# Optimization experiments

Hardware: AMD Instinct MI355X
Metric: run time of the kernel (lower is better)

The kernel has to match this reference:

```python
import jax, jax.numpy as jnp
import numpy as np

EPS = 1e-5

def group_norm(x, num_groups, eps=EPS):
    # x: [B, C, H, W]; no affine (matches F.group_norm with weight=None)
    B, C, H, W = x.shape
    xg = x.reshape(B, num_groups, (C // num_groups) * H * W)
    mean = jnp.mean(xg, axis=-1, keepdims=True)
    var = jnp.var(xg, axis=-1, keepdims=True)
    xg = (xg - mean) * jax.lax.rsqrt(var + eps)
    return xg.reshape(B, C, H, W)

def setup_inputs() -> dict:
    key = jax.random.key(0)
    ks = jax.random.split(key, 5)
    B, C, H, W = 32, 256, 32, 32
    # kaiming-uniform-ish scale for linear weights
    bound = 1.0 / np.sqrt(C)
    x = jax.random.normal(ks[0], (B, C, H, W), dtype=jnp.float32)
    WQ = jax.random.uniform(ks[1], (C, C), jnp.float32, -bound, bound)
    WK = jax.random.uniform(ks[2], (C, C), jnp.float32, -bound, bound)
    WV = jax.random.uniform(ks[3], (C, C), jnp.float32, -bound, bound)
    Wo = jax.random.uniform(ks[4], (C, C), jnp.float32, -bound, bound)
    z = jnp.zeros((C,), jnp.float32)
    return {"x": x, "WQ": WQ, "bQ": z, "WK": WK, "bK": z,
            "WV": WV, "bV": z, "Wo": Wo, "bo": z}

def reference(x, WQ, bQ, WK, bK, WV, bV, Wo, bo):
    B, C, H, W = x.shape
    G = min(32, C)
    h = group_norm(x, G)                      # [B,C,H,W]
    h = h.reshape(B, C, H * W).transpose(0, 2, 1)  # [B, S, C], S = H*W
    q = h @ WQ + bQ
    k = h @ WK + bK
    v = h @ WV + bV
    scale = C ** (-0.5)
    attn = jnp.einsum('bsc,btc->bst', q, k) * scale   # [B,S,S]
    attn = jax.nn.softmax(attn, axis=-1)
    o = jnp.einsum('bst,btc->bsc', attn, v)           # [B,S,C]
    o = o @ Wo + bo                                   # output Nin while in [B,S,C]
    o = o.transpose(0, 2, 1).reshape(B, C, H, W)
    return x + o
```

## Files before the change

kernel.cpp:

```cpp
#include <hip/hip_runtime.h>
#include <stdint.h>

#define BB  32
#define CC  256
#define SS  1024
#define GG  32
#define GCH 8
#define EPS 1e-5f

typedef __attribute__((ext_vector_type(8))) short short8;
typedef __attribute__((ext_vector_type(4))) float f32x4;
typedef __attribute__((ext_vector_type(16))) float f32x16;
typedef unsigned short ushort;

__device__ __forceinline__ float bf2f(ushort u){
  union { unsigned int i; float f; } v; v.i = ((unsigned int)u) << 16; return v.f;
}
__device__ __forceinline__ ushort f2bf(float f){
  union { float f; unsigned int i; } v; v.f = f;
  unsigned int r = v.i + 0x7FFFu + ((v.i >> 16) & 1u);
  return (ushort)(r >> 16);
}
__device__ __forceinline__ unsigned int cvt_pk_bf16(float lo, float hi){
  unsigned int r;
  asm("v_cvt_pk_bf16_f32 %0, %1, %2" : "=v"(r) : "v"(lo), "v"(hi));
  return r;
}

typedef __attribute__((address_space(3))) unsigned int lds_uint;
typedef const __attribute__((address_space(1))) unsigned int glob_uint;
__device__ __forceinline__ void ld_lds16(const void* g, void* l){
  __builtin_amdgcn_global_load_lds((glob_uint*)g, (lds_uint*)l, 16, 0, 0);
}

__global__ __launch_bounds__(256) void sniff_k(const unsigned int* __restrict__ xw,
                                               int* __restrict__ flag)
{
  const int tid = threadIdx.x;
  unsigned int w = xw[tid];
  ushort lo = (ushort)(w & 0xFFFFu);
  int e = (lo >> 7) & 0xFF;
  int ok = (lo == 0 || (e >= 100 && e <= 130)) ? 1 : 0;
  __shared__ int cnt;
  if (tid == 0) cnt = 0;
  __syncthreads();
  atomicAdd(&cnt, ok);
  __syncthreads();
  if (tid == 0) *flag = (cnt > 192) ? 1 : 0;
}

__global__ __launch_bounds__(256) void convert_pre(
    const void* w0, const void* w1, const void* w2, const void* w3,
    const void* b0, const void* b1, const void* b2, const void* b3,
    ushort* __restrict__ WT, float* __restrict__ biasF,
    const int* __restrict__ flag)
{
  const int f = *flag;
  const int z = blockIdx.z;
  const float scl = (z == 0) ? 0.0901684400557f : 1.0f;
  const void* wsel = z==0?w0:z==1?w1:z==2?w2:w3;
  ushort* dst = WT + (long long)z * 65536;
  __shared__ ushort t[64][65];
  const int tid = threadIdx.x;
  const int tx = tid & 63, ty = tid >> 6;
  const int r0 = blockIdx.x * 64, c0 = blockIdx.y * 64;
  for (int j = 0; j < 64; j += 4){
    const int idx = (r0+ty+j)*256 + c0+tx;
    float v = f ? bf2f(((const ushort*)wsel)[idx]) : ((const float*)wsel)[idx];
    t[ty+j][tx] = f2bf(v * scl);
  }
  __syncthreads();
  for (int j = 0; j < 64; j += 4) dst[(c0+ty+j)*256 + r0+tx] = t[tx][ty+j];
  if (blockIdx.x == 0 && blockIdx.y == 0){
    const void* bsel = z==0?b0:z==1?b1:z==2?b2:b3;
    float bv = f ? bf2f(((const ushort*)bsel)[tid]) : ((const float*)bsel)[tid];
    biasF[z*256 + tid] = bv * scl;
  }
}

__global__ __launch_bounds__(256) void gn_stats(const void* __restrict__ x,
                                                float* __restrict__ stats,
                                                const int* __restrict__ flag)
{
  const int f = *flag;
  const int g = blockIdx.x, b = blockIdx.y;
  const int tid = threadIdx.x;
  const long long base = ((long long)b * CC + g * GCH) * SS;
  float sum = 0.f, ss = 0.f;
  if (f){
    const ushort* xg = (const ushort*)x + base;
    #pragma unroll
    for (int j = 0; j < 4; j++){
      uint4 u = *(const uint4*)(xg + (j*256 + tid)*8);
      const ushort* e = (const ushort*)&u;
      #pragma unroll
      for (int i = 0; i < 8; i++){ float v = bf2f(e[i]); sum += v; ss += v*v; }
    }
  } else {
    const float* xg = (const float*)x + base;
    #pragma unroll
    for (int j = 0; j < 8; j++){
      float4 v4 = *(const float4*)(xg + (j*256 + tid)*4);
      sum += v4.x+v4.y+v4.z+v4.w;
      ss  += v4.x*v4.x+v4.y*v4.y+v4.z*v4.z+v4.w*v4.w;
    }
  }
  __shared__ float red[8];
  const int lane = tid & 63, w = tid >> 6;
  #pragma unroll
  for (int o = 32; o > 0; o >>= 1){
    sum += __shfl_down(sum, o);
    ss  += __shfl_down(ss, o);
  }
  if (lane == 0){ red[w] = sum; red[4+w] = ss; }
  __syncthreads();
  if (tid == 0){
    float s1 = red[0]+red[1]+red[2]+red[3];
    float s2 = red[4]+red[5]+red[6]+red[7];
    float mean = s1 / (float)(GCH*SS);
    float var  = s2 / (float)(GCH*SS) - mean*mean;
    const int idx = b*GG + g;
    stats[idx*2]   = mean;
    stats[idx*2+1] = rsqrtf(var + EPS);
  }
}

__global__ __launch_bounds__(256) void gn_norm(const void* __restrict__ x,
                                               ushort* __restrict__ h,
                                               const float* __restrict__ stats,
                                               const int* __restrict__ flag)
{
  const int f = *flag;
  const int c0 = blockIdx.x * 64, s0 = blockIdx.y * 64, b = blockIdx.z;
  const int tid = threadIdx.x;
  __shared__ ushort T[64][72];
  const int row = tid >> 2;
  const int qr  = tid & 3;
  const int g = (c0 + row) >> 3;
  const float mean = stats[(b*GG + g)*2];
  const float rstd = stats[(b*GG + g)*2 + 1];
  const long long xrow = ((long long)b * CC + c0 + row) * SS + s0;
  if (f){
    const ushort* xr = (const ushort*)x + xrow;
    #pragma unroll
    for (int j = 0; j < 2; j++){
      const int col = qr*16 + j*8;
      uint4 u = *(const uint4*)(xr + col);
      const ushort* e = (const ushort*)&u;
      #pragma unroll
      for (int i = 0; i < 8; i++) T[row][col+i] = f2bf((bf2f(e[i]) - mean) * rstd);
    }
  } else {
    const float* xr = (const float*)x + xrow;
    #pragma unroll
    for (int j = 0; j < 4; j++){
      const int col = qr*16 + j*4;
      float4 v4 = *(const float4*)(xr + col);
      T[row][col+0] = f2bf((v4.x - mean) * rstd);
      T[row][col+1] = f2bf((v4.y - mean) * rstd);
      T[row][col+2] = f2bf((v4.z - mean) * rstd);
      T[row][col+3] = f2bf((v4.w - mean) * rstd);
    }
  }
  __syncthreads();
  #pragma unroll
  for (int pass = 0; pass < 2; pass++){
    const int sr = pass*32 + (tid >> 3);
    const int cl = (tid & 7) * 8;
    ushort tmp[8];
    #pragma unroll
    for (int e = 0; e < 8; e++) tmp[e] = T[cl+e][sr];
    *(uint4*)(&h[((long long)b * SS + s0 + sr) * CC + c0 + cl]) = *(const uint4*)tmp;
  }
}

template<int MODE>
__global__ __launch_bounds__(256) void gemm128(
    const ushort* __restrict__ A,
    const ushort* __restrict__ BT,
    ushort* __restrict__ Cmat,
    int lda, int ldb, int ldc, int K,
    long long sA, long long sB, long long sC,
    const float* __restrict__ biasF,
    const void* __restrict__ xres,
    void* __restrict__ outp,
    ushort* __restrict__ vTp,
    long long xoff,
    const int* __restrict__ flag)
{
  extern __shared__ __attribute__((aligned(16))) ushort smem[];
  ushort* As = smem;
  ushort* Bs = smem + 8192;
  const int tid  = threadIdx.x;
  const int lane = tid & 63;
  const int w    = tid >> 6;
  const int wr   = w >> 1, wc = w & 1;
  const int bz   = blockIdx.z;
  const int m0 = blockIdx.x * 128;
  const int n0 = blockIdx.y * 128;

  const int rr = lane & 15;
  const int hi = lane >> 4;
  const int crow = lane >> 3;
  const int pslot = lane & 7;

  f32x4 acc[4][4] = {};

  const ushort* Ab = A + (long long)bz * sA;
  const ushort* Bb = BT + (long long)bz * sB;

  for (int k0 = 0; k0 < K; k0 += 64){
    #pragma unroll
    for (int j = 0; j < 4; j++){
      const int ck = w*4 + j;
      const int r  = ck*8 + crow;
      const int s  = pslot ^ (r & 7);
      ld_lds16(Ab + (long long)(m0 + r) * lda + k0 + s*8, &As[ck * 512]);
    }
    #pragma unroll
    for (int j = 0; j < 4; j++){
      const int ck = w*4 + j;
      const int r  = ck*8 + crow;
      const int s  = pslot ^ (r & 7);
      ld_lds16(Bb + (long long)(n0 + r) * ldb + k0 + s*8, &Bs[ck * 512]);
    }
    asm volatile("s_waitcnt vmcnt(0)" ::: "memory");
    __builtin_amdgcn_sched_barrier(0);
    __syncthreads();

    #pragma unroll
    for (int kk = 0; kk < 2; kk++){
      short8 af[4], bfr[4];
      const int lbyte = kk*64 + hi*16;
      #pragma unroll
      for (int mf = 0; mf < 4; mf++){
        const int row = wr*64 + mf*16 + rr;
        af[mf] = *(const short8*)((const char*)As + row*128 + (lbyte ^ ((row & 7) << 4)));
      }
      #pragma unroll
      for (int nf = 0; nf < 4; nf++){
        const int row = wc*64 + nf*16 + rr;
        bfr[nf] = *(const short8*)((const char*)Bs + row*128 + (lbyte ^ ((row & 7) << 4)));
      }
      #pragma unroll
      for (int mf = 0; mf < 4; mf++)
        #pragma unroll
        for (int nf = 0; nf < 4; nf++)
          acc[mf][nf] = __builtin_amdgcn_mfma_f32_16x16x32_bf16(af[mf], bfr[nf], acc[mf][nf], 0, 0, 0);
    }
    __syncthreads();
  }

  const int rb = 4 * (lane >> 4);
  if (MODE == 0){
    if (bz < 2){
      ushort* Co = Cmat + (long long)bz * sC;
      #pragma unroll
      for (int mf = 0; mf < 4; mf++){
        #pragma unroll
        for (int nf = 0; nf < 4; nf++){
          const int col = n0 + wc*64 + nf*16 + rr;
          const float badd = biasF[bz*256 + col];
          #pragma unroll
          for (int r = 0; r < 4; r++){
            const int row = m0 + wr*64 + mf*16 + rb + r;
            Co[(long long)row * ldc + col] = f2bf(acc[mf][nf][r] + badd);
          }
        }
      }
    } else {
      #pragma unroll
      for (int mf = 0; mf < 4; mf++){
        #pragma unroll
        for (int nf = 0; nf < 4; nf++){
          const int col = n0 + wc*64 + nf*16 + rr;
          const float badd = biasF[512 + col];
          #pragma unroll
          for (int r = 0; r < 4; r++){
            const int row = m0 + wr*64 + mf*16 + rb + r;
            const int bL = row >> 10, s = row & 1023;
            vTp[((long long)bL * CC + col) * SS + s] = f2bf(acc[mf][nf][r] + badd);
          }
        }
      }
    }
  } else {
    const int bL = m0 >> 10;
    const int s0 = m0 & 1023;
    #pragma unroll
    for (int mf = 0; mf < 4; mf++){
      #pragma unroll
      for (int nf = 0; nf < 4; nf++){
        const int colL = wc*64 + nf*16 + rr;
        const float badd = biasF[768 + n0 + colL];
        #pragma unroll
        for (int r = 0; r < 4; r++){
          const int rowL = wr*64 + mf*16 + rb + r;
          smem[colL * 128 + rowL] = f2bf(acc[mf][nf][r] + badd);
        }
      }
    }
    __syncthreads();
    const int f = *flag;
    for (int i = tid; i < 2048; i += 256){
      const int colL = i >> 4;
      const int rowL = (i & 15) * 8;
      const long long oi = xoff + ((long long)bL * CC + n0 + colL) * SS + s0 + rowL;
      const ushort* pu = &smem[colL * 128 + rowL];
      if (f){
        const ushort* xu = (const ushort*)xres + oi;
        ushort* ou = (ushort*)outp + oi;
        ushort tmp[8];
        #pragma unroll
        for (int e = 0; e < 8; e++) tmp[e] = f2bf(bf2f(xu[e]) + bf2f(pu[e]));
        *(uint4*)ou = *(const uint4*)tmp;
      } else {
        const float* xf = (const float*)xres + oi;
        float* of = (float*)outp + oi;
        float4 a0 = *(const float4*)xf;
        float4 a1 = *(const float4*)(xf + 4);
        float4 r0, r1;
        r0.x = a0.x + bf2f(pu[0]); r0.y = a0.y + bf2f(pu[1]);
        r0.z = a0.z + bf2f(pu[2]); r0.w = a0.w + bf2f(pu[3]);
        r1.x = a1.x + bf2f(pu[4]); r1.y = a1.y + bf2f(pu[5]);
        r1.z = a1.z + bf2f(pu[6]); r1.w = a1.w + bf2f(pu[7]);
        *(float4*)of = r0;
        *(float4*)(of + 4) = r1;
      }
    }
  }
}

__global__ __launch_bounds__(512, 1) void attn_fused(
    const ushort* __restrict__ q, const ushort* __restrict__ k,
    const ushort* __restrict__ vT, ushort* __restrict__ oC)
{
  __shared__ ushort Kb[2][64 * 256];
  __shared__ ushort Vb[2][256 * 64];
  const int tid = threadIdx.x, lane = tid & 63, w = tid >> 6;
  const int l31 = lane & 31, hi2 = lane >> 5;
  const int qg = w & 3, ch = w >> 2;
  const int b = blockIdx.x, qt = blockIdx.y;

  const char* kgB = (const char*)(k + (long long)b * SS * CC);
  const char* vgB = (const char*)(vT + (long long)b * CC * SS);
  const int qrow = qt*128 + qg*32 + l31;
  const ushort* qgp = q + ((long long)b * SS + qrow) * CC + hi2*8;
  ushort* ogq = oC + ((long long)b * SS + qrow) * CC + ch*128;

  short8 qf[16];
  #pragma unroll
  for (int kk = 0; kk < 16; kk++)
    qf[kk] = *(const short8*)(qgp + kk*16);

  f32x16 Oa[4] = {};
  float mrow = -1e30f, lrow = 0.0f;

  #define STAGE(buf, t0)                                                        \
  {                                                                             \
    _Pragma("unroll")                                                           \
    for (int j = 0; j < 4; j++){                                                \
      const int ck = j*8 + w;                                                   \
      const int tr = ck*2 + (lane >> 5);                                        \
      const int xb = ((lane & 31) * 16) ^ ((tr & 31) << 4);                     \
      ld_lds16(kgB + (long long)((t0) + tr) * 512 + xb, &Kb[buf][ck * 512]);    \
    }                                                                           \
    _Pragma("unroll")                                                           \
    for (int j = 0; j < 4; j++){                                                \
      const int ck = j*8 + w;                                                   \
      const int vr = ck*2 + (lane >> 5);                                        \
      const int u  = (lane & 31) ^ ((vr & 7) << 2);                             \
      const int vc = vr*4 + (u & 3);                                            \
      const int tb = (u >> 2) * 16;                                             \
      ld_lds16(vgB + (long long)vc * 2048 + (t0)*2 + tb, &Vb[buf][ck * 512]);   \
    }                                                                           \
  }

  STAGE(0, 0);
  asm volatile("s_waitcnt vmcnt(0)" ::: "memory");
  __builtin_amdgcn_sched_barrier(0);
  __syncthreads();

  const int coff = hi2 * 16;
  const int kswz = l31 << 4;

  for (int t = 0; t < 16; t++){
    const int cur = t & 1;
    if (t < 15) STAGE(cur ^ 1, (t+1)*64);

    f32x16 Sa0 = {}, Sa1 = {};
    __builtin_amdgcn_s_setprio(1);
    #pragma unroll
    for (int kk = 0; kk < 16; kk++){
      const int off = kk*32 + coff;
      short8 ka0 = *(const short8*)((const char*)&Kb[cur][0] + l31*512 + (off ^ kswz));
      short8 ka1 = *(const short8*)((const char*)&Kb[cur][0] + (32 + l31)*512 + (off ^ kswz));
      Sa0 = __builtin_amdgcn_mfma_f32_32x32x16_bf16(ka0, qf[kk], Sa0, 0, 0, 0);
      Sa1 = __builtin_amdgcn_mfma_f32_32x32x16_bf16(ka1, qf[kk], Sa1, 0, 0, 0);
    }
    __builtin_amdgcn_s_setprio(0);

    float mx = Sa0[0];
    #pragma unroll
    for (int r = 1; r < 16; r++) mx = fmaxf(mx, Sa0[r]);
    #pragma unroll
    for (int r = 0; r < 16; r++) mx = fmaxf(mx, Sa1[r]);
    mx = fmaxf(mx, __shfl_xor(mx, 32));
    if (!__all(mx <= mrow + 8.0f)){
      const float mn = fmaxf(mrow, mx);
      const float sc = __builtin_amdgcn_exp2f(mrow - mn);
      mrow = mn;
      lrow *= sc;
      #pragma unroll
      for (int nf = 0; nf < 4; nf++)
        #pragma unroll
        for (int r = 0; r < 16; r++) Oa[nf][r] *= sc;
    }
    float rs = 0.0f;
    #pragma unroll
    for (int r = 0; r < 16; r++){
      Sa0[r] = __builtin_amdgcn_exp2f(Sa0[r] - mrow); rs += Sa0[r];
      Sa1[r] = __builtin_amdgcn_exp2f(Sa1[r] - mrow); rs += Sa1[r];
    }
    rs += __shfl_xor(rs, 32);
    lrow += rs;

    __builtin_amdgcn_s_setprio(1);
    #pragma unroll
    for (int g = 0; g < 4; g++){
      unsigned int b0, b1, b2, b3;
      if (g < 2){
        b0 = cvt_pk_bf16(Sa0[(g&1)*8+0], Sa0[(g&1)*8+1]);
        b1 = cvt_pk_bf16(Sa0[(g&1)*8+2], Sa0[(g&1)*8+3]);
        b2 = cvt_pk_bf16(Sa0[(g&1)*8+4], Sa0[(g&1)*8+5]);
        b3 = cvt_pk_bf16(Sa0[(g&1)*8+6], Sa0[(g&1)*8+7]);
      } else {
        b0 = cvt_pk_bf16(Sa1[(g&1)*8+0], Sa1[(g&1)*8+1]);
        b1 = cvt_pk_bf16(Sa1[(g&1)*8+2], Sa1[(g&1)*8+3]);
        b2 = cvt_pk_bf16(Sa1[(g&1)*8+4], Sa1[(g&1)*8+5]);
        b3 = cvt_pk_bf16(Sa1[(g&1)*8+6], Sa1[(g&1)*8+7]);
      }
      unsigned int s0 = (unsigned int)__shfl_xor((int)b0, 32);
      unsigned int s1 = (unsigned int)__shfl_xor((int)b1, 32);
      unsigned int s2 = (unsigned int)__shfl_xor((int)b2, 32);
      unsigned int s3 = (unsigned int)__shfl_xor((int)b3, 32);
      union { uint4 u; short8 s; } pw;
      pw.u.x = hi2 ? s2 : b0;
      pw.u.y = hi2 ? s3 : b1;
      pw.u.z = hi2 ? b2 : s0;
      pw.u.w = hi2 ? b3 : s1;
      const short8 pb = pw.s;
      const int G = g*2 + hi2;
      #pragma unroll
      for (int nf = 0; nf < 4; nf++){
        const int c = ch*128 + nf*32 + l31;
        const int vr = c >> 2;
        const int slot = (((G << 2) | (c & 3)) ^ ((vr & 7) << 2));
        short8 va = *(const short8*)((const char*)&Vb[cur][0] + vr*512 + slot*16);
        Oa[nf] = __builtin_amdgcn_mfma_f32_32x32x16_bf16(va, pb, Oa[nf], 0, 0, 0);
      }
    }
    __builtin_amdgcn_s_setprio(0);

    asm volatile("s_waitcnt vmcnt(0)" ::: "memory");
    __builtin_amdgcn_sched_barrier(0);
    __syncthreads();
  }
  #undef STAGE

  const float inv = 1.0f / lrow;
  #pragma unroll
  for (int nf = 0; nf < 4; nf++){
    #pragma unroll
    for (int g = 0; g < 4; g++){
      uint2 ov;
      ov.x = cvt_pk_bf16(Oa[nf][g*4+0] * inv, Oa[nf][g*4+1] * inv);
      ov.y = cvt_pk_bf16(Oa[nf][g*4+2] * inv, Oa[nf][g*4+3] * inv);
      *(uint2*)(ogq + nf*32 + g*8 + hi2*4) = ov;
    }
  }
}

extern "C" void kernel_launch(void* const* d_in, const int* in_sizes, int n_in,
                              void* d_out, int out_size, void* d_ws, size_t ws_size,
                              hipStream_t stream)
{
  (void)in_sizes; (void)n_in; (void)out_size;
  const void* x  = d_in[0];
  const void* WQ = d_in[1];
  const void* bQ = d_in[2];
  const void* WK = d_in[3];
  const void* bK = d_in[4];
  const void* WV = d_in[5];
  const void* bV = d_in[6];
  const void* Wo = d_in[7];
  const void* bo = d_in[8];

  const long long NE  = (long long)BB * SS * CC;
  const long long SC  = (long long)SS * CC;

  uint8_t* base = (uint8_t*)d_ws;
  int* flag          = (int*)base;
  float* biasF       = (float*)(base + 256);
  float* stats       = (float*)(base + 256 + 4096);
  ushort* WT         = (ushort*)(base + 256 + 4096 + 8192);
  ushort* h          = WT + 4 * 65536;

  const long long fixedB = 256 + 4096 + 8192 + 4LL*65536*2 + NE*2;
  int CB = 1;
  for (int c = 32; c >= 1; c >>= 1){
    if (fixedB + 4LL * c * SC * 2 <= (long long)ws_size){ CB = c; break; }
  }

  ushort* q  = h + NE;
  ushort* k  = q + (long long)CB * SC;
  ushort* vT = k + (long long)CB * SC;
  ushort* oC = vT + (long long)CB * SC;

  dim3 blk(256);
  const size_t shmem = 32768;

  sniff_k<<<1, blk, 0, stream>>>((const unsigned int*)x, flag);
  convert_pre<<<dim3(4, 4, 4), blk, 0, stream>>>(WQ, WK, WV, Wo, bQ, bK, bV, bo, WT, biasF, flag);
  gn_stats<<<dim3(GG, BB), blk, 0, stream>>>(x, stats, flag);
  gn_norm<<<dim3(4, 16, BB), blk, 0, stream>>>(x, h, stats, flag);

  for (int c0 = 0; c0 < BB; c0 += CB){
    const ushort* hC = h + (long long)c0 * SC;
    gemm128<0><<<dim3(CB*8, 2, 3), blk, shmem, stream>>>(
        hC, WT, q, CC, CC, CC, CC,
        0LL, 65536LL, (long long)CB * SC,
        biasF, nullptr, nullptr, vT, 0LL, flag);
    attn_fused<<<dim3(CB, 8), dim3(512), 0, stream>>>(q, k, vT, oC);
    gemm128<3><<<dim3(CB*8, 2, 1), blk, shmem, stream>>>(
        oC, WT + 3*65536, nullptr, CC, CC, SS, CC,
        0LL, 0LL, 0LL,
        biasF, x, d_out, nullptr, (long long)c0 * SC, flag);
  }
}
```

Before: 151.2 us.

## Split attention work across key halves instead of channel halves, merge via LDS

The attention kernel's two wave halves now each process half of every 64-key tile (32 keys) across all 256 output channels, instead of each computing all 64 keys' scores and splitting channels. This removes the duplicated QK^T MFMA work and the duplicated exp/max work across the two channel halves. The cost is double the O accumulator registers per wave (8 f32x16 fragments). There is also a final split-softmax merge: one half writes its partial O, max and sum to LDS, reusing the K/V buffers, and the other half combines and stores them. Higher register pressure could hurt scheduling.

```diff
diff --git a/kernel.cpp b/kernel.cpp
--- a/kernel.cpp
+++ b/kernel.cpp
@@ -337,6 +337,8 @@
 {
   __shared__ ushort Kb[2][64 * 256];
   __shared__ ushort Vb[2][256 * 64];
+  __shared__ float  Mb[8][32];
+  __shared__ float  Lb[8][32];
   const int tid = threadIdx.x, lane = tid & 63, w = tid >> 6;
   const int l31 = lane & 31, hi2 = lane >> 5;
   const int qg = w & 3, ch = w >> 2;
@@ -346,14 +348,14 @@
   const char* vgB = (const char*)(vT + (long long)b * CC * SS);
   const int qrow = qt*128 + qg*32 + l31;
   const ushort* qgp = q + ((long long)b * SS + qrow) * CC + hi2*8;
-  ushort* ogq = oC + ((long long)b * SS + qrow) * CC + ch*128;
+  ushort* ogq = oC + ((long long)b * SS + qrow) * CC;
 
   short8 qf[16];
   #pragma unroll
   for (int kk = 0; kk < 16; kk++)
     qf[kk] = *(const short8*)(qgp + kk*16);
 
-  f32x16 Oa[4] = {};
+  f32x16 Oa[8] = {};
   float mrow = -1e30f, lrow = 0.0f;
 
   #define STAGE(buf, t0)                                                        \
@@ -383,28 +385,25 @@
 
   const int coff = hi2 * 16;
   const int kswz = l31 << 4;
+  const int krow = ch*32 + l31;
 
   for (int t = 0; t < 16; t++){
     const int cur = t & 1;
     if (t < 15) STAGE(cur ^ 1, (t+1)*64);
 
-    f32x16 Sa0 = {}, Sa1 = {};
+    f32x16 Sa = {};
     __builtin_amdgcn_s_setprio(1);
     #pragma unroll
     for (int kk = 0; kk < 16; kk++){
       const int off = kk*32 + coff;
-      short8 ka0 = *(const short8*)((const char*)&Kb[cur][0] + l31*512 + (off ^ kswz));
-      short8 ka1 = *(const short8*)((const char*)&Kb[cur][0] + (32 + l31)*512 + (off ^ kswz));
-      Sa0 = __builtin_amdgcn_mfma_f32_32x32x16_bf16(ka0, qf[kk], Sa0, 0, 0, 0);
-      Sa1 = __builtin_amdgcn_mfma_f32_32x32x16_bf16(ka1, qf[kk], Sa1, 0, 0, 0);
+      short8 ka = *(const short8*)((const char*)&Kb[cur][0] + krow*512 + (off ^ kswz));
+      Sa = __builtin_amdgcn_mfma_f32_32x32x16_bf16(ka, qf[kk], Sa, 0, 0, 0);
     }
     __builtin_amdgcn_s_setprio(0);
 
-    float mx = Sa0[0];
-    #pragma unroll
-    for (int r = 1; r < 16; r++) mx = fmaxf(mx, Sa0[r]);
-    #pragma unroll
-    for (int r = 0; r < 16; r++) mx = fmaxf(mx, Sa1[r]);
+    float mx = Sa[0];
+    #pragma unroll
+    for (int r = 1; r < 16; r++) mx = fmaxf(mx, Sa[r]);
     mx = fmaxf(mx, __shfl_xor(mx, 32));
     if (!__all(mx <= mrow + 8.0f)){
       const float mn = fmaxf(mrow, mx);
@@ -412,34 +411,25 @@
       mrow = mn;
       lrow *= sc;
       #pragma unroll
-      for (int nf = 0; nf < 4; nf++)
+      for (int nf = 0; nf < 8; nf++)
         #pragma unroll
         for (int r = 0; r < 16; r++) Oa[nf][r] *= sc;
     }
     float rs = 0.0f;
     #pragma unroll
     for (int r = 0; r < 16; r++){
-      Sa0[r] = __builtin_amdgcn_exp2f(Sa0[r] - mrow); rs += Sa0[r];
-      Sa1[r] = __builtin_amdgcn_exp2f(Sa1[r] - mrow); rs += Sa1[r];
+      Sa[r] = __builtin_amdgcn_exp2f(Sa[r] - mrow); rs += Sa[r];
     }
     rs += __shfl_xor(rs, 32);
     lrow += rs;
 
     __builtin_amdgcn_s_setprio(1);
     #pragma unroll
-    for (int g = 0; g < 4; g++){
-      unsigned int b0, b1, b2, b3;
-      if (g < 2){
-        b0 = cvt_pk_bf16(Sa0[(g&1)*8+0], Sa0[(g&1)*8+1]);
-        b1 = cvt_pk_bf16(Sa0[(g&1)*8+2], Sa0[(g&1)*8+3]);
-        b2 = cvt_pk_bf16(Sa0[(g&1)*8+4], Sa0[(g&1)*8+5]);
-        b3 = cvt_pk_bf16(Sa0[(g&1)*8+6], Sa0[(g&1)*8+7]);
-      } else {
-        b0 = cvt_pk_bf16(Sa1[(g&1)*8+0], Sa1[(g&1)*8+1]);
-        b1 = cvt_pk_bf16(Sa1[(g&1)*8+2], Sa1[(g&1)*8+3]);
-        b2 = cvt_pk_bf16(Sa1[(g&1)*8+4], Sa1[(g&1)*8+5]);
-        b3 = cvt_pk_bf16(Sa1[(g&1)*8+6], Sa1[(g&1)*8+7]);
-      }
+    for (int g = 0; g < 2; g++){
+      unsigned int b0 = cvt_pk_bf16(Sa[g*8+0], Sa[g*8+1]);
+      unsigned int b1 = cvt_pk_bf16(Sa[g*8+2], Sa[g*8+3]);
+      unsigned int b2 = cvt_pk_bf16(Sa[g*8+4], Sa[g*8+5]);
+      unsigned int b3 = cvt_pk_bf16(Sa[g*8+6], Sa[g*8+7]);
       unsigned int s0 = (unsigned int)__shfl_xor((int)b0, 32);
       unsigned int s1 = (unsigned int)__shfl_xor((int)b1, 32);
       unsigned int s2 = (unsigned int)__shfl_xor((int)b2, 32);
@@ -450,10 +440,10 @@
       pw.u.z = hi2 ? b2 : s0;
       pw.u.w = hi2 ? b3 : s1;
       const short8 pb = pw.s;
-      const int G = g*2 + hi2;
-      #pragma unroll
-      for (int nf = 0; nf < 4; nf++){
-        const int c = ch*128 + nf*32 + l31;
+      const int G = ch*4 + g*2 + hi2;
+      #pragma unroll
+      for (int nf = 0; nf < 8; nf++){
+        const int c = nf*32 + l31;
         const int vr = c >> 2;
         const int slot = (((G << 2) | (c & 3)) ^ ((vr & 7) << 2));
         short8 va = *(const short8*)((const char*)&Vb[cur][0] + vr*512 + slot*16);
@@ -468,15 +458,39 @@
   }
   #undef STAGE
 
-  const float inv = 1.0f / lrow;
-  #pragma unroll
-  for (int nf = 0; nf < 4; nf++){
-    #pragma unroll
-    for (int g = 0; g < 4; g++){
-      uint2 ov;
-      ov.x = cvt_pk_bf16(Oa[nf][g*4+0] * inv, Oa[nf][g*4+1] * inv);
-      ov.y = cvt_pk_bf16(Oa[nf][g*4+2] * inv, Oa[nf][g*4+3] * inv);
-      *(uint2*)(ogq + nf*32 + g*8 + hi2*4) = ov;
+  float* Ob = (qg < 2) ? (float*)&Kb[qg][0] : (float*)&Vb[qg - 2][0];
+  if (ch == 1){
+    #pragma unroll
+    for (int nf = 0; nf < 8; nf++){
+      #pragma unroll
+      for (int r = 0; r < 16; r++){
+        const int c = nf*32 + (r & 3) + 8*(r >> 2) + 4*hi2;
+        Ob[c*32 + l31] = Oa[nf][r];
+      }
+    }
+    if (hi2 == 0){ Mb[w][l31] = mrow; Lb[w][l31] = lrow; }
+  }
+  __syncthreads();
+  if (ch == 0){
+    const float m2 = Mb[w + 4][l31], l2 = Lb[w + 4][l31];
+    const float mx = fmaxf(mrow, m2);
+    const float f1 = __builtin_amdgcn_exp2f(mrow - mx);
+    const float f2 = __builtin_amdgcn_exp2f(m2 - mx);
+    const float inv = 1.0f / (f1*lrow + f2*l2);
+    const float a1 = f1 * inv, a2 = f2 * inv;
+    #pragma unroll
+    for (int nf = 0; nf < 8; nf++){
+      #pragma unroll
+      for (int g = 0; g < 4; g++){
+        float o0 = Oa[nf][g*4+0]*a1 + Ob[(nf*32 + g*8 + hi2*4 + 0)*32 + l31]*a2;
+        float o1 = Oa[nf][g*4+1]*a1 + Ob[(nf*32 + g*8 + hi2*4 + 1)*32 + l31]*a2;
+        float o2 = Oa[nf][g*4+2]*a1 + Ob[(nf*32 + g*8 + hi2*4 + 2)*32 + l31]*a2;
+        float o3 = Oa[nf][g*4+3]*a1 + Ob[(nf*32 + g*8 + hi2*4 + 3)*32 + l31]*a2;
+        uint2 ov;
+        ov.x = cvt_pk_bf16(o0, o1);
+        ov.y = cvt_pk_bf16(o2, o3);
+        *(uint2*)(ogq + nf*32 + g*8 + hi2*4) = ov;
+      }
     }
   }
 }
```

After: 140.7 us. 7.0% less time.
